# Performance work log

Hardware: AMD Instinct MI355X
Metric: run time of the kernel (lower is better)

The kernel has to match this reference:

```python
import jax, jax.numpy as jnp
import numpy as np

B, S, D, F, E, SH, K = 2, 2048, 2048, 1024, 16, 2, 2


def setup_inputs() -> dict:
    key = jax.random.key(0)
    ks = jax.random.split(key, 8)
    std = 0.02
    mk = lambda k, sh: (jax.random.normal(k, sh, jnp.float32) * std)
    return {
        "x": jax.random.normal(ks[0], (B, S, D), jnp.float32),
        "wa": mk(ks[1], (D, E)),                      # router, no bias
        "rg": mk(ks[2], (E, D, F)), "rgb": jnp.zeros((E, F), jnp.float32),
        "rw1": mk(ks[3], (E, D, F)), "rb1": jnp.zeros((E, F), jnp.float32),
        "rw2": mk(ks[4], (E, F, D)), "rb2": jnp.zeros((E, D), jnp.float32),
        "sg": mk(ks[5], (SH, D, F)), "sgb": jnp.zeros((SH, F), jnp.float32),
        "sw1": mk(ks[6], (SH, D, F)), "sb1": jnp.zeros((SH, F), jnp.float32),
        "sw2": mk(ks[7], (SH, F, D)), "sb2": jnp.zeros((SH, D), jnp.float32),
    }


def _experts_all(x, g, gb, w1, b1, w2, b2):
    """Run every expert in the stack on every token.
    x: [b,s,d]; g,w1: [e,d,f]; w2: [e,f,d] -> out [b,s,e,d].
    Expert: w2( gelu(gated(x)) * w1(x) ). torch GELU default = exact erf.
    """
    y = jax.nn.gelu(jnp.einsum('bsd,edf->bsef', x, g) + gb, approximate=False)
    y = y * (jnp.einsum('bsd,edf->bsef', x, w1) + b1)
    return jnp.einsum('bsef,efd->bsed', y, w2) + b2


def reference(x, wa, rg, rgb, rw1, rb1, rw2, rb2, sg, sgb, sw1, sb1, sw2, sb2):
    # sigmoid affinity router + top-k, renormalized over the k selected
    aff = jax.nn.sigmoid(jnp.einsum('bsd,de->bse', x, wa))
    topk_p, topk_i = jax.lax.top_k(aff, K)                   # [b,s,k]
    topk_p = topk_p / jnp.sum(topk_p, axis=-1, keepdims=True)
    # dense combine weights [b,s,E]; zero for unselected experts, so the
    # masked-scatter of the original is reproduced exactly by a weighted sum
    combine = jnp.sum(jax.nn.one_hot(topk_i, E, dtype=x.dtype) * topk_p[..., None], axis=2)
    routed = jnp.einsum('bsed,bse->bsd',
                        _experts_all(x, rg, rgb, rw1, rb1, rw2, rb2), combine)
    shared = jnp.sum(_experts_all(x, sg, sgb, sw1, sb1, sw2, sb2), axis=2)
    return x + shared + routed
```

## Files before the change

### kernel.cpp

```cpp
#include <hip/hip_runtime.h>
#include <hip/hip_bf16.h>
#include <math.h>

typedef __bf16 bf16;
typedef bf16  bf16x8 __attribute__((ext_vector_type(8)));
typedef bf16  bf16x4 __attribute__((ext_vector_type(4)));
typedef float f32x4  __attribute__((ext_vector_type(4)));

#define TOKENS 4096
#define DM 2048
#define FF 1024
#define NE 16
#define SH_BASE 12288
#define BK 64

#define WS_CNT    0
#define WS_POS    64
#define WS_BASE   128
#define WS_TOPKW  256
#define WS_TOPKI  33024
#define WS_TSLOT  65792
#define WS_LIST   98560
#define WS_XB     180480
#define WS_H      16957696
#define WS_Y      58900736
#define WS_B1R    142786816
#define WS_B1S    277004544
#define WS_W2TR   293781760
#define WS_W2TS   360890624

__device__ __forceinline__ bf16 f2bf(float f) {
  unsigned u = __builtin_bit_cast(unsigned, f);
  u += 0x7fffu + ((u >> 16) & 1u);
  unsigned short h = (unsigned short)(u >> 16);
  return __builtin_bit_cast(bf16, h);
}

typedef const __attribute__((address_space(1))) void* gas_t;
typedef __attribute__((address_space(3))) void* las_t;
__device__ __forceinline__ void load_lds16(const bf16* g, bf16* l) {
  __builtin_amdgcn_global_load_lds((gas_t)g, (las_t)l, 16, 0, 0);
}

__global__ void cvt_x_kernel(const float* __restrict__ x, bf16* __restrict__ xb) {
  const size_t idx = ((size_t)blockIdx.x * 256 + threadIdx.x) * 4;
  f32x4 v = *(const f32x4*)(x + idx);
  bf16x4 o;
  o[0] = f2bf(v[0]); o[1] = f2bf(v[1]); o[2] = f2bf(v[2]); o[3] = f2bf(v[3]);
  *(bf16x4*)(xb + idx) = o;
}

__global__ void transpose_cvt_kernel(const float* __restrict__ in, bf16* __restrict__ out,
                                     int R, int C) {
  __shared__ float tile[64][65];
  const size_t zo = (size_t)blockIdx.z * R * C;
  const int c0 = blockIdx.x * 64, r0 = blockIdx.y * 64;
  const int t = threadIdx.x;
  const int lr = t >> 2;
  const int lc = (t & 3) * 4;
  const float* src = in + zo + (size_t)(r0 + lr) * C + c0;
#pragma unroll
  for (int j = 0; j < 4; j++) {
    const f32x4 v = *(const f32x4*)(src + lc + j * 16);
    tile[lr][lc + j * 16 + 0] = v[0];
    tile[lr][lc + j * 16 + 1] = v[1];
    tile[lr][lc + j * 16 + 2] = v[2];
    tile[lr][lc + j * 16 + 3] = v[3];
  }
  __syncthreads();
  const int co = t >> 4;
  const int ro = (t & 15) * 4;
#pragma unroll
  for (int j = 0; j < 4; j++) {
    const int c = co + j * 16;
    bf16x4 v;
    v[0] = f2bf(tile[ro + 0][c]);
    v[1] = f2bf(tile[ro + 1][c]);
    v[2] = f2bf(tile[ro + 2][c]);
    v[3] = f2bf(tile[ro + 3][c]);
    *(bf16x4*)(out + zo + (size_t)(c0 + c) * R + r0 + ro) = v;
  }
}

__global__ void transpose_cvt_fused_kernel(const float* __restrict__ in, bf16* __restrict__ out,
                                           int half) {
  __shared__ float tile[64][65];
  const size_t zi = (size_t)blockIdx.z * DM * FF;
  const size_t zo = (size_t)blockIdx.z * (2 * FF) * DM;
  const int c0 = blockIdx.x * 64, r0 = blockIdx.y * 64;
  const int t = threadIdx.x;
  const int lr = t >> 2;
  const int lc = (t & 3) * 4;
  const float* src = in + zi + (size_t)(r0 + lr) * FF + c0;
#pragma unroll
  for (int j = 0; j < 4; j++) {
    const f32x4 v = *(const f32x4*)(src + lc + j * 16);
    tile[lr][lc + j * 16 + 0] = v[0];
    tile[lr][lc + j * 16 + 1] = v[1];
    tile[lr][lc + j * 16 + 2] = v[2];
    tile[lr][lc + j * 16 + 3] = v[3];
  }
  __syncthreads();
  const int co = t >> 4;
  const int ro = (t & 15) * 4;
#pragma unroll
  for (int j = 0; j < 4; j++) {
    const int c = co + j * 16;
    const int f = c0 + c;
    const int fr = ((f >> 4) << 5) + half * 16 + (f & 15);
    bf16x4 v;
    v[0] = f2bf(tile[ro + 0][c]);
    v[1] = f2bf(tile[ro + 1][c]);
    v[2] = f2bf(tile[ro + 2][c]);
    v[3] = f2bf(tile[ro + 3][c]);
    *(bf16x4*)(out + zo + (size_t)fr * DM + r0 + ro) = v;
  }
}

#define RT_TOK 16
#define RT_DK  256
#define RT_PITCH (RT_DK + 4)

__global__ __launch_bounds__(256) void router_kernel(
    const float* __restrict__ x, const float* __restrict__ wa,
    float* __restrict__ topk_w, int* __restrict__ topk_i,
    int* __restrict__ cnt) {
  __shared__ float xs[RT_TOK][RT_PITCH];
  __shared__ float was[NE][RT_PITCH];
  __shared__ float aff[RT_TOK][17];

  const int tid = threadIdx.x;
  const int t = tid >> 4;
  const int e = tid & 15;
  const int t0 = blockIdx.x * RT_TOK;

  f32x4 acc4 = {0.f, 0.f, 0.f, 0.f};

  for (int d0 = 0; d0 < DM; d0 += RT_DK) {
    __syncthreads();
    {
      const int r = tid >> 4;
      const int c4 = (tid & 15) * 4;
      const float* src = x + (size_t)(t0 + r) * DM + d0;
#pragma unroll
      for (int j = 0; j < 4; j++)
        *(f32x4*)(&xs[r][c4 + j * 64]) = *(const f32x4*)(src + c4 + j * 64);
    }
    {
      const int e2 = tid & 15;
      const int dd = (tid >> 4) * 16;
#pragma unroll
      for (int j = 0; j < 16; j++)
        was[e2][dd + j] = wa[(size_t)(d0 + dd + j) * NE + e2];
    }
    __syncthreads();
#pragma unroll 16
    for (int d = 0; d < RT_DK; d += 4) {
      const f32x4 xv = *(const f32x4*)(&xs[t][d]);
      const f32x4 wv = *(const f32x4*)(&was[e][d]);
      acc4 += xv * wv;
    }
  }

  const float a = acc4[0] + acc4[1] + acc4[2] + acc4[3];
  aff[t][e] = 1.f / (1.f + expf(-a));
  __syncthreads();

  if (e == 0) {
    float b0 = -1e30f, b1 = -1e30f; int i0 = 0, i1 = 0;
    for (int i = 0; i < NE; i++) {
      const float v = aff[t][i];
      if (v > b0) { b1 = b0; i1 = i0; b0 = v; i0 = i; }
      else if (v > b1) { b1 = v; i1 = i; }
    }
    const int tok = t0 + t;
    const float inv = 1.f / (b0 + b1);
    topk_w[tok * 2] = b0 * inv;  topk_w[tok * 2 + 1] = b1 * inv;
    topk_i[tok * 2] = i0;        topk_i[tok * 2 + 1] = i1;
    atomicAdd(&cnt[i0], 1);      atomicAdd(&cnt[i1], 1);
  }
}

__global__ void prefix_kernel(const int* __restrict__ cnt, int* __restrict__ base) {
  if (threadIdx.x == 0) {
    int acc = 0;
    for (int e = 0; e < NE; e++) { base[e] = acc; acc += (cnt[e] + 127) & ~127; }
    base[NE] = SH_BASE;
    base[NE + 1] = SH_BASE + TOKENS;
  }
}

__global__ void build_lists_kernel(const int* __restrict__ topk_i, const int* __restrict__ base,
                                   int* __restrict__ pos, int* __restrict__ list,
                                   int* __restrict__ token_slot) {
  const int t = blockIdx.x * 256 + threadIdx.x;
  if (t >= TOKENS) return;
#pragma unroll
  for (int k = 0; k < 2; k++) {
    const int e = topk_i[t * 2 + k];
    const int p = atomicAdd(&pos[e], 1);
    const int slot = base[e] + p;
    list[slot] = t;
    token_slot[t * 2 + k] = slot;
  }
  list[SH_BASE + t] = t;
  list[SH_BASE + TOKENS + t] = t;
}

#define GEMM_GRID_MAX 2304

__device__ __forceinline__ bool map_tile(int flat, const int* __restrict__ cnt,
                                         int& e, int& my, int& nx) {
  int o = 0;
  for (int ee = 0; ee < NE + 2; ++ee) {
    const int ce = (ee < NE) ? cnt[ee] : TOKENS;
    const int me = (ce + 127) >> 7;
    const int Te = me << 4;
    if (flat < o + Te) {
      const int l = flat - o;
      const int s = (l & 7) * (me << 1) + (l >> 3);
      nx = s / me;
      my = s - nx * me;
      e = ee;
      return true;
    }
    o += Te;
  }
  return false;
}

__global__ __launch_bounds__(256, 2) void gemm1_kernel(
    const bf16* __restrict__ xb, const int* __restrict__ list,
    const int* __restrict__ base, const int* __restrict__ cnt,
    const bf16* __restrict__ B1R, const bf16* __restrict__ B1S,
    const float* __restrict__ rgb, const float* __restrict__ rb1,
    const float* __restrict__ sgb, const float* __restrict__ sb1,
    bf16* __restrict__ H) {
  int e, bmy, bnx;
  if (!map_tile(blockIdx.x, cnt, e, bmy, bnx)) return;
  const int ce = (e < NE) ? cnt[e] : TOKENS;
  const int m0 = bmy * 128;
  const int n0 = bnx * 128;
  const int bse = base[e];

  const bf16* B1; const float *gb, *ub;
  if (e < NE) { B1 = B1R + (size_t)e * (2 * FF) * DM; gb = rgb + e * FF; ub = rb1 + e * FF; }
  else { const int s = e - NE; B1 = B1S + (size_t)s * (2 * FF) * DM; gb = sgb + s * FF; ub = sb1 + s * FF; }

  __shared__ bf16 As[2][128 * BK];
  __shared__ bf16 Bs[2][128 * BK];

  const int tid = threadIdx.x, lane = tid & 63, wid = tid >> 6;
  const int lrow = lane >> 3;
  const int laneK = (((lane & 7) ^ lrow) << 3);
  const int q0 = wid << 5;

  const bf16* aP[4];
#pragma unroll
  for (int i = 0; i < 4; i++) {
    int rA = m0 + q0 + (i << 3) + lrow;
    if (rA >= ce) rA = ce - 1;
    aP[i] = xb + (size_t)list[bse + rA] * DM + laneK;
  }
  const bf16* bP = B1 + (size_t)(n0 + q0 + lrow) * DM + laneK;

  const int wm = (wid & 1) * 64, wn = (wid >> 1) * 64;
  const int m16 = lane & 15, quad = lane >> 4, xor7 = m16 & 7;

  f32x4 acc[4][4] = {};

#pragma unroll
  for (int i = 0; i < 4; i++) {
    load_lds16(aP[i], &As[0][(q0 + (i << 3)) * BK + (lane << 3)]);
    load_lds16(bP + (size_t)(i * 8) * DM, &Bs[0][(q0 + (i << 3)) * BK + (lane << 3)]);
  }

  int cur = 0;
  for (int k0 = 0; k0 < DM; k0 += BK) {
    __syncthreads();
    if (k0 + BK < DM) {
      const int nxt = cur ^ 1;
      const int kn = k0 + BK;
#pragma unroll
      for (int i = 0; i < 4; i++) {
        load_lds16(aP[i] + kn, &As[nxt][(q0 + (i << 3)) * BK + (lane << 3)]);
        load_lds16(bP + (size_t)(i * 8) * DM + kn, &Bs[nxt][(q0 + (i << 3)) * BK + (lane << 3)]);
      }
    }
#pragma unroll
    for (int kk = 0; kk < 2; kk++) {
      const int slot = (((kk << 2) + quad) ^ xor7) << 3;
      bf16x8 af[4], bfr[4];
#pragma unroll
      for (int i = 0; i < 4; i++) {
        af[i]  = *(const bf16x8*)(&As[cur][(wm + m16 + 16 * i) * BK + slot]);
        bfr[i] = *(const bf16x8*)(&Bs[cur][(wn + m16 + 16 * i) * BK + slot]);
      }
#pragma unroll
      for (int mi = 0; mi < 4; mi++)
#pragma unroll
        for (int ni = 0; ni < 4; ni++)
          acc[mi][ni] = __builtin_amdgcn_mfma_f32_16x16x32_bf16(af[mi], bfr[ni], acc[mi][ni], 0, 0, 0);
    }
    cur ^= 1;
  }

  const int q4 = quad * 4;
  const int fbase = ((n0 + wn) >> 1) + m16;
#pragma unroll
  for (int mi = 0; mi < 4; mi++) {
#pragma unroll
    for (int nj = 0; nj < 2; nj++) {
      const int f = fbase + nj * 16;
      const float gbv = gb[f], ubv = ub[f];
#pragma unroll
      for (int r = 0; r < 4; r++) {
        const int row = m0 + wm + mi * 16 + q4 + r;
        const float g = acc[mi][2 * nj][r] + gbv;
        const float u = acc[mi][2 * nj + 1][r] + ubv;
        const float h = 0.5f * g * (1.f + erff(g * 0.70710678118f)) * u;
        H[(size_t)(bse + row) * FF + f] = f2bf(h);
      }
    }
  }
}

__global__ __launch_bounds__(256, 2) void gemm2_kernel(
    const bf16* __restrict__ Hb, const int* __restrict__ base, const int* __restrict__ cnt,
    const bf16* __restrict__ rw2T, const bf16* __restrict__ sw2T,
    const float* __restrict__ rb2, const float* __restrict__ sb2,
    bf16* __restrict__ Y) {
  int e, bmy, bnx;
  if (!map_tile(blockIdx.x, cnt, e, bmy, bnx)) return;
  const int m0 = bmy * 128;
  const int n0 = bnx * 128;
  const int bse = base[e];

  const bf16* B; const float* bb;
  if (e < NE) { B = rw2T + (size_t)e * DM * FF; bb = rb2 + e * DM; }
  else { const int s = e - NE; B = sw2T + (size_t)s * DM * FF; bb = sb2 + s * DM; }

  __shared__ bf16 As[2][128 * BK];
  __shared__ bf16 Bs[2][128 * BK];

  const int tid = threadIdx.x, lane = tid & 63, wid = tid >> 6;
  const int lrow = lane >> 3;
  const int laneK = (((lane & 7) ^ lrow) << 3);
  const int q0 = wid << 5;

  const bf16* aP = Hb + (size_t)(bse + m0 + q0 + lrow) * FF + laneK;
  const bf16* bP = B  + (size_t)(n0 + q0 + lrow) * FF + laneK;

  const int wm = (wid & 1) * 64, wn = (wid >> 1) * 64;
  const int m16 = lane & 15, quad = lane >> 4, xor7 = m16 & 7;

  f32x4 acc[4][4] = {};

#pragma unroll
  for (int i = 0; i < 4; i++) {
    load_lds16(aP + (size_t)(i * 8) * FF, &As[0][(q0 + (i << 3)) * BK + (lane << 3)]);
    load_lds16(bP + (size_t)(i * 8) * FF, &Bs[0][(q0 + (i << 3)) * BK + (lane << 3)]);
  }

  int cur = 0;
  for (int k0 = 0; k0 < FF; k0 += BK) {
    __syncthreads();
    if (k0 + BK < FF) {
      const int nxt = cur ^ 1;
      const int kn = k0 + BK;
#pragma unroll
      for (int i = 0; i < 4; i++) {
        load_lds16(aP + (size_t)(i * 8) * FF + kn, &As[nxt][(q0 + (i << 3)) * BK + (lane << 3)]);
        load_lds16(bP + (size_t)(i * 8) * FF + kn, &Bs[nxt][(q0 + (i << 3)) * BK + (lane << 3)]);
      }
    }
#pragma unroll
    for (int kk = 0; kk < 2; kk++) {
      const int slot = (((kk << 2) + quad) ^ xor7) << 3;
      bf16x8 af[4], bfr[4];
#pragma unroll
      for (int i = 0; i < 4; i++) {
        af[i]  = *(const bf16x8*)(&As[cur][(wm + m16 + 16 * i) * BK + slot]);
        bfr[i] = *(const bf16x8*)(&Bs[cur][(wn + m16 + 16 * i) * BK + slot]);
      }
#pragma unroll
      for (int mi = 0; mi < 4; mi++)
#pragma unroll
        for (int ni = 0; ni < 4; ni++)
          acc[mi][ni] = __builtin_amdgcn_mfma_f32_16x16x32_bf16(af[mi], bfr[ni], acc[mi][ni], 0, 0, 0);
    }
    cur ^= 1;
  }

  const int q4 = quad * 4;
#pragma unroll
  for (int mi = 0; mi < 4; mi++) {
#pragma unroll
    for (int ni = 0; ni < 4; ni++) {
      const int n = n0 + wn + ni * 16 + m16;
      const float bv = bb[n];
#pragma unroll
      for (int r = 0; r < 4; r++) {
        const int row = m0 + wm + mi * 16 + q4 + r;
        Y[(size_t)(bse + row) * DM + n] = f2bf(acc[mi][ni][r] + bv);
      }
    }
  }
}

__global__ void combine_kernel(const float* __restrict__ x, const bf16* __restrict__ Y,
                               const int* __restrict__ token_slot, const float* __restrict__ topk_w,
                               float* __restrict__ out) {
  const int t = blockIdx.x;
  const int d = threadIdx.x * 8;
  const int s0 = token_slot[t * 2], s1 = token_slot[t * 2 + 1];
  const float w0 = topk_w[t * 2], w1 = topk_w[t * 2 + 1];
  const bf16x8 ya = *(const bf16x8*)(Y + (size_t)(SH_BASE + t) * DM + d);
  const bf16x8 yb = *(const bf16x8*)(Y + (size_t)(SH_BASE + TOKENS + t) * DM + d);
  const bf16x8 y0 = *(const bf16x8*)(Y + (size_t)s0 * DM + d);
  const bf16x8 y1 = *(const bf16x8*)(Y + (size_t)s1 * DM + d);
  const float* xp = x + (size_t)t * DM + d;
  float* op = out + (size_t)t * DM + d;
#pragma unroll
  for (int j = 0; j < 8; j++)
    op[j] = xp[j] + (float)ya[j] + (float)yb[j] + w0 * (float)y0[j] + w1 * (float)y1[j];
}

extern "C" void kernel_launch(void* const* d_in, const int* in_sizes, int n_in,
                              void* d_out, int out_size, void* d_ws, size_t ws_size,
                              hipStream_t stream) {
  (void)in_sizes; (void)n_in; (void)out_size; (void)ws_size;
  const float* x   = (const float*)d_in[0];
  const float* wa  = (const float*)d_in[1];
  const float* rg  = (const float*)d_in[2];
  const float* rgb = (const float*)d_in[3];
  const float* rw1 = (const float*)d_in[4];
  const float* rb1 = (const float*)d_in[5];
  const float* rw2 = (const float*)d_in[6];
  const float* rb2 = (const float*)d_in[7];
  const float* sg  = (const float*)d_in[8];
  const float* sgb = (const float*)d_in[9];
  const float* sw1 = (const float*)d_in[10];
  const float* sb1 = (const float*)d_in[11];
  const float* sw2 = (const float*)d_in[12];
  const float* sb2 = (const float*)d_in[13];
  float* out = (float*)d_out;

  char* ws = (char*)d_ws;
  int*   cnt        = (int*)(ws + WS_CNT);
  int*   pos        = (int*)(ws + WS_POS);
  int*   basep      = (int*)(ws + WS_BASE);
  float* topk_w     = (float*)(ws + WS_TOPKW);
  int*   topk_i     = (int*)(ws + WS_TOPKI);
  int*   token_slot = (int*)(ws + WS_TSLOT);
  int*   list       = (int*)(ws + WS_LIST);
  bf16*  xb         = (bf16*)(ws + WS_XB);
  bf16*  H          = (bf16*)(ws + WS_H);
  bf16*  Y          = (bf16*)(ws + WS_Y);
  bf16*  B1R        = (bf16*)(ws + WS_B1R);
  bf16*  B1S        = (bf16*)(ws + WS_B1S);
  bf16*  W2TR       = (bf16*)(ws + WS_W2TR);
  bf16*  W2TS       = (bf16*)(ws + WS_W2TS);

  hipMemsetAsync(ws, 0, 128, stream);

  cvt_x_kernel<<<(TOKENS * DM) / 1024, 256, 0, stream>>>(x, xb);
  router_kernel<<<TOKENS / RT_TOK, 256, 0, stream>>>(x, wa, topk_w, topk_i, cnt);
  prefix_kernel<<<1, 64, 0, stream>>>(cnt, basep);
  build_lists_kernel<<<TOKENS / 256, 256, 0, stream>>>(topk_i, basep, pos, list, token_slot);

  transpose_cvt_fused_kernel<<<dim3(FF / 64, DM / 64, NE), 256, 0, stream>>>(rg,  B1R, 0);
  transpose_cvt_fused_kernel<<<dim3(FF / 64, DM / 64, NE), 256, 0, stream>>>(rw1, B1R, 1);
  transpose_cvt_fused_kernel<<<dim3(FF / 64, DM / 64, 2),  256, 0, stream>>>(sg,  B1S, 0);
  transpose_cvt_fused_kernel<<<dim3(FF / 64, DM / 64, 2),  256, 0, stream>>>(sw1, B1S, 1);
  transpose_cvt_kernel<<<dim3(DM / 64, FF / 64, NE), 256, 0, stream>>>(rw2, W2TR, FF, DM);
  transpose_cvt_kernel<<<dim3(DM / 64, FF / 64, 2),  256, 0, stream>>>(sw2, W2TS, FF, DM);

  gemm1_kernel<<<GEMM_GRID_MAX, 256, 0, stream>>>(
      xb, list, basep, cnt, B1R, B1S, rgb, rb1, sgb, sb1, H);
  gemm2_kernel<<<GEMM_GRID_MAX, 256, 0, stream>>>(
      H, basep, cnt, W2TR, W2TS, rb2, sb2, Y);
  combine_kernel<<<TOKENS, 256, 0, stream>>>(x, Y, token_slot, topk_w, out);
}
```

Baseline: 920.8 us.

## Enlarge GEMM tiles to 128x256 with 8 waves and triple-buffered LDS pipeline

Both expert GEMMs now use 128x256 tiles computed by 512-thread blocks (8 waves, each still owning a 64x64 sub-tile). The LDS double buffer becomes a three-stage ring with explicit vmcnt waits and raw s_barrier, so two K-slices are in flight while one is consumed. MFMA sections are wrapped in s_setprio. The aim is to hide global-load latency and halve the number of tiles, which reduces redundant A-operand traffic. In exchange the blocks need much more LDS (144KB) and run at one block per CU, and the grouped swizzle in the tile mapping is dropped.

```diff
diff --git a/kernel.cpp b/kernel.cpp
--- a/kernel.cpp
+++ b/kernel.cpp
@@ -13,6 +13,8 @@
 #define NE 16
 #define SH_BASE 12288
 #define BK 64
+#define BM 128
+#define BN 256
 
 #define WS_CNT    0
 #define WS_POS    64
@@ -207,20 +209,19 @@
   list[SH_BASE + TOKENS + t] = t;
 }
 
-#define GEMM_GRID_MAX 2304
-
-__device__ __forceinline__ bool map_tile(int flat, const int* __restrict__ cnt,
-                                         int& e, int& my, int& nx) {
+#define GEMM_GRID_MAX 1152
+
+__device__ __forceinline__ bool map_tile8(int flat, const int* __restrict__ cnt,
+                                          int& e, int& my, int& nx) {
   int o = 0;
   for (int ee = 0; ee < NE + 2; ++ee) {
     const int ce = (ee < NE) ? cnt[ee] : TOKENS;
     const int me = (ce + 127) >> 7;
-    const int Te = me << 4;
+    const int Te = me << 3;
     if (flat < o + Te) {
       const int l = flat - o;
-      const int s = (l & 7) * (me << 1) + (l >> 3);
-      nx = s / me;
-      my = s - nx * me;
+      nx = l & 7;
+      my = l >> 3;
       e = ee;
       return true;
     }
@@ -229,7 +230,8 @@
   return false;
 }
 
-__global__ __launch_bounds__(256, 2) void gemm1_kernel(
+
+__global__ __launch_bounds__(512, 1) void gemm1_kernel(
     const bf16* __restrict__ xb, const int* __restrict__ list,
     const int* __restrict__ base, const int* __restrict__ cnt,
     const bf16* __restrict__ B1R, const bf16* __restrict__ B1S,
@@ -237,64 +239,74 @@
     const float* __restrict__ sgb, const float* __restrict__ sb1,
     bf16* __restrict__ H) {
   int e, bmy, bnx;
-  if (!map_tile(blockIdx.x, cnt, e, bmy, bnx)) return;
+  if (!map_tile8(blockIdx.x, cnt, e, bmy, bnx)) return;
   const int ce = (e < NE) ? cnt[e] : TOKENS;
-  const int m0 = bmy * 128;
-  const int n0 = bnx * 128;
+  const int m0 = bmy * BM;
+  const int n0 = bnx * BN;
   const int bse = base[e];
 
   const bf16* B1; const float *gb, *ub;
   if (e < NE) { B1 = B1R + (size_t)e * (2 * FF) * DM; gb = rgb + e * FF; ub = rb1 + e * FF; }
   else { const int s = e - NE; B1 = B1S + (size_t)s * (2 * FF) * DM; gb = sgb + s * FF; ub = sb1 + s * FF; }
 
-  __shared__ bf16 As[2][128 * BK];
-  __shared__ bf16 Bs[2][128 * BK];
+  __shared__ alignas(16) bf16 As[3 * BM * BK];
+  __shared__ alignas(16) bf16 Bs[3 * BN * BK];
 
   const int tid = threadIdx.x, lane = tid & 63, wid = tid >> 6;
   const int lrow = lane >> 3;
-  const int laneK = (((lane & 7) ^ lrow) << 3);
-  const int q0 = wid << 5;
-
-  const bf16* aP[4];
-#pragma unroll
-  for (int i = 0; i < 4; i++) {
-    int rA = m0 + q0 + (i << 3) + lrow;
-    if (rA >= ce) rA = ce - 1;
-    aP[i] = xb + (size_t)list[bse + rA] * DM + laneK;
-  }
-  const bf16* bP = B1 + (size_t)(n0 + q0 + lrow) * DM + laneK;
+  const int swz = (((lane & 7) ^ lrow) << 3);
+  const int w8 = wid << 3;
+  const int l8 = lane << 3;
+
+  int ra0 = m0 + w8 + lrow;       if (ra0 >= ce) ra0 = ce - 1;
+  int ra1 = m0 + 64 + w8 + lrow;  if (ra1 >= ce) ra1 = ce - 1;
+  const bf16* aSrc0 = xb + (size_t)list[bse + ra0] * DM + swz;
+  const bf16* aSrc1 = xb + (size_t)list[bse + ra1] * DM + swz;
+  const bf16* bSrc0 = B1 + (size_t)(n0 + w8 + lrow) * DM + swz;
+  const bf16* bSrc1 = B1 + (size_t)(n0 + 64 + w8 + lrow) * DM + swz;
+  const bf16* bSrc2 = B1 + (size_t)(n0 + 128 + w8 + lrow) * DM + swz;
+  const bf16* bSrc3 = B1 + (size_t)(n0 + 192 + w8 + lrow) * DM + swz;
 
   const int wm = (wid & 1) * 64, wn = (wid >> 1) * 64;
   const int m16 = lane & 15, quad = lane >> 4, xor7 = m16 & 7;
 
   f32x4 acc[4][4] = {};
 
-#pragma unroll
-  for (int i = 0; i < 4; i++) {
-    load_lds16(aP[i], &As[0][(q0 + (i << 3)) * BK + (lane << 3)]);
-    load_lds16(bP + (size_t)(i * 8) * DM, &Bs[0][(q0 + (i << 3)) * BK + (lane << 3)]);
-  }
-
+#define G1_STAGE(b, kof)                                         \
+  {                                                              \
+    bf16* Ab = As + (b) * (BM * BK);                             \
+    bf16* Bb = Bs + (b) * (BN * BK);                             \
+    load_lds16(aSrc0 + (kof), Ab + w8 * BK + l8);                \
+    load_lds16(aSrc1 + (kof), Ab + (64 + w8) * BK + l8);         \
+    load_lds16(bSrc0 + (kof), Bb + w8 * BK + l8);                \
+    load_lds16(bSrc1 + (kof), Bb + (64 + w8) * BK + l8);         \
+    load_lds16(bSrc2 + (kof), Bb + (128 + w8) * BK + l8);        \
+    load_lds16(bSrc3 + (kof), Bb + (192 + w8) * BK + l8);        \
+  }
+
+  G1_STAGE(0, 0)
+  G1_STAGE(1, BK)
+  asm volatile("s_waitcnt vmcnt(6)" ::: "memory");
+  __builtin_amdgcn_s_barrier();
+
+  const int NT = DM / BK;
   int cur = 0;
-  for (int k0 = 0; k0 < DM; k0 += BK) {
-    __syncthreads();
-    if (k0 + BK < DM) {
-      const int nxt = cur ^ 1;
-      const int kn = k0 + BK;
-#pragma unroll
-      for (int i = 0; i < 4; i++) {
-        load_lds16(aP[i] + kn, &As[nxt][(q0 + (i << 3)) * BK + (lane << 3)]);
-        load_lds16(bP + (size_t)(i * 8) * DM + kn, &Bs[nxt][(q0 + (i << 3)) * BK + (lane << 3)]);
-      }
-    }
+  for (int t = 0; t < NT; ++t) {
+    if (t + 2 < NT) {
+      int nb = cur + 2; if (nb >= 3) nb -= 3;
+      G1_STAGE(nb, (t + 2) * BK)
+    }
+    const bf16* Ab = As + cur * (BM * BK);
+    const bf16* Bb = Bs + cur * (BN * BK);
+    __builtin_amdgcn_s_setprio(1);
 #pragma unroll
     for (int kk = 0; kk < 2; kk++) {
       const int slot = (((kk << 2) + quad) ^ xor7) << 3;
       bf16x8 af[4], bfr[4];
 #pragma unroll
       for (int i = 0; i < 4; i++) {
-        af[i]  = *(const bf16x8*)(&As[cur][(wm + m16 + 16 * i) * BK + slot]);
-        bfr[i] = *(const bf16x8*)(&Bs[cur][(wn + m16 + 16 * i) * BK + slot]);
+        af[i]  = *(const bf16x8*)(Ab + (wm + m16 + 16 * i) * BK + slot);
+        bfr[i] = *(const bf16x8*)(Bb + (wn + m16 + 16 * i) * BK + slot);
       }
 #pragma unroll
       for (int mi = 0; mi < 4; mi++)
@@ -302,8 +314,13 @@
         for (int ni = 0; ni < 4; ni++)
           acc[mi][ni] = __builtin_amdgcn_mfma_f32_16x16x32_bf16(af[mi], bfr[ni], acc[mi][ni], 0, 0, 0);
     }
-    cur ^= 1;
-  }
+    __builtin_amdgcn_s_setprio(0);
+    if (t < NT - 2)       asm volatile("s_waitcnt vmcnt(6)" ::: "memory");
+    else if (t == NT - 2) asm volatile("s_waitcnt vmcnt(0)" ::: "memory");
+    if (t < NT - 1) __builtin_amdgcn_s_barrier();
+    cur = (cur + 1 == 3) ? 0 : cur + 1;
+  }
+#undef G1_STAGE
 
   const int q4 = quad * 4;
   const int fbase = ((n0 + wn) >> 1) + m16;
@@ -325,63 +342,77 @@
   }
 }
 
-__global__ __launch_bounds__(256, 2) void gemm2_kernel(
+__global__ __launch_bounds__(512, 1) void gemm2_kernel(
     const bf16* __restrict__ Hb, const int* __restrict__ base, const int* __restrict__ cnt,
     const bf16* __restrict__ rw2T, const bf16* __restrict__ sw2T,
     const float* __restrict__ rb2, const float* __restrict__ sb2,
     bf16* __restrict__ Y) {
   int e, bmy, bnx;
-  if (!map_tile(blockIdx.x, cnt, e, bmy, bnx)) return;
-  const int m0 = bmy * 128;
-  const int n0 = bnx * 128;
+  if (!map_tile8(blockIdx.x, cnt, e, bmy, bnx)) return;
+  const int m0 = bmy * BM;
+  const int n0 = bnx * BN;
   const int bse = base[e];
 
   const bf16* B; const float* bb;
   if (e < NE) { B = rw2T + (size_t)e * DM * FF; bb = rb2 + e * DM; }
   else { const int s = e - NE; B = sw2T + (size_t)s * DM * FF; bb = sb2 + s * DM; }
 
-  __shared__ bf16 As[2][128 * BK];
-  __shared__ bf16 Bs[2][128 * BK];
+  __shared__ alignas(16) bf16 As[3 * BM * BK];
+  __shared__ alignas(16) bf16 Bs[3 * BN * BK];
 
   const int tid = threadIdx.x, lane = tid & 63, wid = tid >> 6;
   const int lrow = lane >> 3;
-  const int laneK = (((lane & 7) ^ lrow) << 3);
-  const int q0 = wid << 5;
-
-  const bf16* aP = Hb + (size_t)(bse + m0 + q0 + lrow) * FF + laneK;
-  const bf16* bP = B  + (size_t)(n0 + q0 + lrow) * FF + laneK;
+  const int swz = (((lane & 7) ^ lrow) << 3);
+  const int w8 = wid << 3;
+  const int l8 = lane << 3;
+
+  const bf16* aSrc0 = Hb + (size_t)(bse + m0 + w8 + lrow) * FF + swz;
+  const bf16* aSrc1 = Hb + (size_t)(bse + m0 + 64 + w8 + lrow) * FF + swz;
+  const bf16* bSrc0 = B + (size_t)(n0 + w8 + lrow) * FF + swz;
+  const bf16* bSrc1 = B + (size_t)(n0 + 64 + w8 + lrow) * FF + swz;
+  const bf16* bSrc2 = B + (size_t)(n0 + 128 + w8 + lrow) * FF + swz;
+  const bf16* bSrc3 = B + (size_t)(n0 + 192 + w8 + lrow) * FF + swz;
 
   const int wm = (wid & 1) * 64, wn = (wid >> 1) * 64;
   const int m16 = lane & 15, quad = lane >> 4, xor7 = m16 & 7;
 
   f32x4 acc[4][4] = {};
 
-#pragma unroll
-  for (int i = 0; i < 4; i++) {
-    load_lds16(aP + (size_t)(i * 8) * FF, &As[0][(q0 + (i << 3)) * BK + (lane << 3)]);
-    load_lds16(bP + (size_t)(i * 8) * FF, &Bs[0][(q0 + (i << 3)) * BK + (lane << 3)]);
-  }
-
+#define G2_STAGE(b, kof)                                         \
+  {                                                              \
+    bf16* Ab = As + (b) * (BM * BK);                             \
+    bf16* Bb = Bs + (b) * (BN * BK);                             \
+    load_lds16(aSrc0 + (kof), Ab + w8 * BK + l8);                \
+    load_lds16(aSrc1 + (kof), Ab + (64 + w8) * BK + l8);         \
+    load_lds16(bSrc0 + (kof), Bb + w8 * BK + l8);                \
+    load_lds16(bSrc1 + (kof), Bb + (64 + w8) * BK + l8);         \
+    load_lds16(bSrc2 + (kof), Bb + (128 + w8) * BK + l8);        \
+    load_lds16(bSrc3 + (kof), Bb + (192 + w8) * BK + l8);        \
+  }
+
+  G2_STAGE(0, 0)
+  G2_STAGE(1, BK)
+  asm volatile("s_waitcnt vmcnt(6)" ::: "memory");
+  __builtin_amdgcn_s_barrier();
+
+  const int NT = FF / BK;
   int cur = 0;
-  for (int k0 = 0; k0 < FF; k0 += BK) {
-    __syncthreads();
-    if (k0 + BK < FF) {
-      const int nxt = cur ^ 1;
-      const int kn = k0 + BK;
-#pragma unroll
-      for (int i = 0; i < 4; i++) {
-        load_lds16(aP + (size_t)(i * 8) * FF + kn, &As[nxt][(q0 + (i << 3)) * BK + (lane << 3)]);
-        load_lds16(bP + (size_t)(i * 8) * FF + kn, &Bs[nxt][(q0 + (i << 3)) * BK + (lane << 3)]);
-      }
-    }
+  for (int t = 0; t < NT; ++t) {
+    if (t + 2 < NT) {
+      int nb = cur + 2; if (nb >= 3) nb -= 3;
+      G2_STAGE(nb, (t + 2) * BK)
+    }
+    const bf16* Ab = As + cur * (BM * BK);
+    const bf16* Bb = Bs + cur * (BN * BK);
+    __builtin_amdgcn_s_setprio(1);
 #pragma unroll
     for (int kk = 0; kk < 2; kk++) {
       const int slot = (((kk << 2) + quad) ^ xor7) << 3;
       bf16x8 af[4], bfr[4];
 #pragma unroll
       for (int i = 0; i < 4; i++) {
-        af[i]  = *(const bf16x8*)(&As[cur][(wm + m16 + 16 * i) * BK + slot]);
-        bfr[i] = *(const bf16x8*)(&Bs[cur][(wn + m16 + 16 * i) * BK + slot]);
+        af[i]  = *(const bf16x8*)(Ab + (wm + m16 + 16 * i) * BK + slot);
+        bfr[i] = *(const bf16x8*)(Bb + (wn + m16 + 16 * i) * BK + slot);
       }
 #pragma unroll
       for (int mi = 0; mi < 4; mi++)
@@ -389,8 +420,13 @@
         for (int ni = 0; ni < 4; ni++)
           acc[mi][ni] = __builtin_amdgcn_mfma_f32_16x16x32_bf16(af[mi], bfr[ni], acc[mi][ni], 0, 0, 0);
     }
-    cur ^= 1;
-  }
+    __builtin_amdgcn_s_setprio(0);
+    if (t < NT - 2)       asm volatile("s_waitcnt vmcnt(6)" ::: "memory");
+    else if (t == NT - 2) asm volatile("s_waitcnt vmcnt(0)" ::: "memory");
+    if (t < NT - 1) __builtin_amdgcn_s_barrier();
+    cur = (cur + 1 == 3) ? 0 : cur + 1;
+  }
+#undef G2_STAGE
 
   const int q4 = quad * 4;
 #pragma unroll
@@ -476,9 +512,9 @@
   transpose_cvt_kernel<<<dim3(DM / 64, FF / 64, NE), 256, 0, stream>>>(rw2, W2TR, FF, DM);
   transpose_cvt_kernel<<<dim3(DM / 64, FF / 64, 2),  256, 0, stream>>>(sw2, W2TS, FF, DM);
 
-  gemm1_kernel<<<GEMM_GRID_MAX, 256, 0, stream>>>(
+  gemm1_kernel<<<GEMM_GRID_MAX, 512, 0, stream>>>(
       xb, list, basep, cnt, B1R, B1S, rgb, rb1, sgb, sb1, H);
-  gemm2_kernel<<<GEMM_GRID_MAX, 256, 0, stream>>>(
+  gemm2_kernel<<<GEMM_GRID_MAX, 512, 0, stream>>>(
       H, basep, cnt, W2TR, W2TS, rb2, sb2, Y);
   combine_kernel<<<TOKENS, 256, 0, stream>>>(x, Y, token_slot, topk_w, out);
 }
```

After: 990.8 us. +7.6%, slower.
